# Kernel tuning notes

Hardware: AMD Instinct MI355X
Metric: run time of the kernel (lower is better)

## Reference

```python
import jax, jax.numpy as jnp
import numpy as np

E, EDGE, MEM = 32768, 128, 128
IN = EDGE + 2 * MEM              # 384
HID = 512
NK = 64                          # num_kernels
KNOTS = 16                       # grid_size
ORDER = 3                        # spline order (cubic)
COEF = KNOTS + ORDER             # 19 basis functions per input dim

# Uniform knot grid on [-1, 1], extended by ORDER knots on each side
_H = 2.0 / KNOTS
GRID = (jnp.arange(-ORDER, KNOTS + ORDER + 1, dtype=jnp.float32) * _H - 1.0)


def _b_splines(x, grid):
    """Cox-de Boor B-spline bases. x: [B, IN] -> [B, IN, COEF]."""
    xe = x[..., None]                                   # [B, IN, 1]
    bases = ((xe >= grid[:-1]) & (xe < grid[1:])).astype(x.dtype)
    for p in range(1, ORDER + 1):
        left = (xe - grid[:-(p + 1)]) / (grid[p:-1] - grid[:-(p + 1)])
        right = (grid[p + 1:] - xe) / (grid[p + 1:] - grid[1:-p])
        bases = left * bases[..., :-1] + right * bases[..., 1:]
    return bases                                        # [B, IN, COEF]


def setup_inputs() -> dict:
    key = jax.random.key(0)
    ks = jax.random.split(key, 7)
    z = jax.random.normal(ks[0], (E, EDGE), jnp.float32)
    mem_src = jax.random.normal(ks[1], (E, MEM), jnp.float32)
    mem_dst = jax.random.normal(ks[2], (E, MEM), jnp.float32)
    base_weight = jax.random.normal(ks[3], (HID, IN), jnp.float32) / np.sqrt(IN)
    spline_weight = jax.random.normal(ks[4], (HID, IN, COEF), jnp.float32) * 0.1
    lin_w = jax.random.normal(ks[5], (NK, HID), jnp.float32) / np.sqrt(HID)
    lin_b = jax.random.normal(ks[6], (NK,), jnp.float32) * 0.01
    return {"z": z, "mem_src": mem_src, "mem_dst": mem_dst,
            "base_weight": base_weight, "spline_weight": spline_weight,
            "lin_w": lin_w, "lin_b": lin_b}


def reference(z, mem_src, mem_dst, base_weight, spline_weight, lin_w, lin_b):
    # concat + tanh squashing (inputs into the [-1,1] knot grid), fp32 math
    x = jnp.tanh(jnp.concatenate([z, mem_src, mem_dst], axis=-1)).astype(jnp.float32)
    # KANLinear: base path (silu residual) + spline path
    bases = _b_splines(x, GRID)                          # [E, IN, COEF]
    h = (jnp.dot(jax.nn.silu(x), base_weight.T)
         + jnp.einsum('bik,oik->bo', bases, spline_weight))  # [E, HID]
    h = jnp.tanh(h)                                      # act='tanh'; dropout=0 -> identity
    return jnp.dot(h, lin_w.T) + lin_b                   # [E, NK]
```

## Files before the change

kernel.cpp:

```cpp
#include <hip/hip_runtime.h>
#include <hip/hip_bf16.h>
#include <cstdint>

#define DI __device__ __forceinline__

using bf16x8 = __attribute__((ext_vector_type(8))) short;
using f32x4  = __attribute__((ext_vector_type(4))) float;

constexpr int IN_DIM = 384;
constexpr int HID    = 512;
constexpr int KTOT   = IN_DIM * 20;
constexpr int BM = 64, BN = 256, BK = 160;
constexpr int NSTEP = KTOT / BK;
constexpr int A_STRIDE_B = 320;
constexpr int A_BYTES    = BM * A_STRIDE_B;
constexpr int LDS_BYTES  = 2 * A_BYTES;

DI unsigned short f2bf(float f) {
  union { float f; uint32_t u; } v; v.f = f;
  uint32_t r = (v.u + 0x7FFFu + ((v.u >> 16) & 1u)) >> 16;
  return (unsigned short)r;
}
DI float fast_tanh(float x) {
  float e = __expf(2.0f * x);
  return 1.0f - 2.0f / (e + 1.0f);
}
DI uint32_t swzw(uint32_t L) { return L ^ ((L >> 6) & 0x70u); }

__global__ __launch_bounds__(256) void kpack(const float* __restrict__ bw,
                                             const float* __restrict__ sw,
                                             unsigned short* __restrict__ Wf) {
  int idx = blockIdx.x * 256 + threadIdx.x;
  int o = idx / IN_DIM;
  int i = idx - o * IN_DIM;
  const float* sp = sw + (size_t)idx * 19;
  const uint32_t gq  = (uint32_t)(o >> 4);
  const uint32_t l16o = (uint32_t)(o & 15);
#pragma unroll
  for (int c = 0; c < 20; ++c) {
    int k = i * 20 + c;
    uint32_t q  = (uint32_t)k >> 5;
    uint32_t kr = (uint32_t)k & 31u;
    uint32_t lane = l16o + ((kr >> 3) << 4);
    uint32_t off = (q * 32u + gq) * 512u + lane * 8u + (kr & 7u);
    float v = (c == 0) ? bw[idx] : sp[c - 1];
    Wf[off] = f2bf(v);
  }
}

__global__ __launch_bounds__(256, 4) void kgemm1(const float* __restrict__ z,
                                                 const float* __restrict__ ms,
                                                 const float* __restrict__ md,
                                                 const unsigned short* __restrict__ Wf,
                                                 unsigned short* __restrict__ hout) {
  extern __shared__ char ldsbuf[];

  const int tid  = threadIdx.x;
  const int lane = tid & 63;
  const int wv   = tid >> 6;
  const int wc   = wv & 3;
  const int l16  = lane & 15;
  const int lhi  = lane >> 4;

  int wg = blockIdx.x;
  int id = (wg & 7) * 128 + (wg >> 3);
  const int mblk = id & 511;
  const int nblk = id >> 9;
  const int row0 = mblk * BM;
  const int col0 = nblk * BN;

  const unsigned short* bpt = Wf + (size_t)(nblk * 16 + wc * 4) * 512 + (size_t)lane * 8;

  const int isl = tid & 7;
  const int arow0 = tid >> 3;
  const uint32_t fw = ((uint32_t)arow0 & 7u) << 4;

  const uint32_t fA = (uint32_t)(l16 & 7) << 4;
  const uint32_t rA = (uint32_t)l16 * A_STRIDE_B + (uint32_t)lhi * 16u;

  f32x4 acc[4][4] = {};

  float xv0, xv1;
  {
    const float* xcol = z + isl;
    float x0 = xcol[(size_t)(row0 + arow0) * 128];
    float x1 = xcol[(size_t)(row0 + arow0 + 32) * 128];
#pragma unroll
    for (int r = 0; r < 2; ++r) {
      float x = (r == 0) ? x0 : x1;
      int arow = arow0 + r * 32;
      float xt = fast_tanh(x);
      float tt = (xt + 1.0f) * 8.0f;
      int   m  = (int)tt; m = m > 16 ? 16 : m;
      float u  = tt - (float)m;
      float omu = 1.0f - u;
      float u2 = u * u, u3 = u2 * u;
      float w0 = omu * omu * omu * (1.0f / 6.0f);
      float w1 = (3.0f * u3 - 6.0f * u2 + 4.0f) * (1.0f / 6.0f);
      float w2 = (-3.0f * u3 + 3.0f * u2 + 3.0f * u + 1.0f) * (1.0f / 6.0f);
      float w3 = u3 * (1.0f / 6.0f);
      float sil = xt / (1.0f + __expf(-xt));
      uint32_t base = (uint32_t)arow * A_STRIDE_B + (uint32_t)isl * 40u;
#pragma unroll
      for (int zz = 0; zz < 5; ++zz)
        *(uint64_t*)(ldsbuf + ((base + zz * 8) ^ fw)) = 0ull;
      *(short*)(ldsbuf + (base ^ fw)) = (short)f2bf(sil);
      *(short*)(ldsbuf + ((base + 2u * (m + 1)) ^ fw)) = (short)f2bf(w0);
      *(short*)(ldsbuf + ((base + 2u * (m + 2)) ^ fw)) = (short)f2bf(w1);
      *(short*)(ldsbuf + ((base + 2u * (m + 3)) ^ fw)) = (short)f2bf(w2);
      if (m < 16)
        *(short*)(ldsbuf + ((base + 2u * (m + 4)) ^ fw)) = (short)f2bf(w3);
    }
    const float* xc1 = z + (8 + isl);
    xv0 = xc1[(size_t)(row0 + arow0) * 128];
    xv1 = xc1[(size_t)(row0 + arow0 + 32) * 128];
  }
  __syncthreads();

  for (int s = 0; s < NSTEP; ++s) {
    const uint32_t pc = (uint32_t)(s & 1);
    const uint32_t pn = pc ^ 1u;
    char* An = ldsbuf + pn * (uint32_t)A_BYTES;
    const char* Ac = ldsbuf + pc * (uint32_t)A_BYTES;

    float xn0 = 0.f, xn1 = 0.f;
    if (s + 1 < NSTEP) {
#pragma unroll
      for (int r = 0; r < 2; ++r) {
        float x = (r == 0) ? xv0 : xv1;
        int arow = arow0 + r * 32;
        float xt = fast_tanh(x);
        float tt = (xt + 1.0f) * 8.0f;
        int   m  = (int)tt; m = m > 16 ? 16 : m;
        float u  = tt - (float)m;
        float omu = 1.0f - u;
        float u2 = u * u, u3 = u2 * u;
        float w0 = omu * omu * omu * (1.0f / 6.0f);
        float w1 = (3.0f * u3 - 6.0f * u2 + 4.0f) * (1.0f / 6.0f);
        float w2 = (-3.0f * u3 + 3.0f * u2 + 3.0f * u + 1.0f) * (1.0f / 6.0f);
        float w3 = u3 * (1.0f / 6.0f);
        float sil = xt / (1.0f + __expf(-xt));
        uint32_t base = (uint32_t)arow * A_STRIDE_B + (uint32_t)isl * 40u;
#pragma unroll
        for (int zz = 0; zz < 5; ++zz)
          *(uint64_t*)(An + ((base + zz * 8) ^ fw)) = 0ull;
        *(short*)(An + (base ^ fw)) = (short)f2bf(sil);
        *(short*)(An + ((base + 2u * (m + 1)) ^ fw)) = (short)f2bf(w0);
        *(short*)(An + ((base + 2u * (m + 2)) ^ fw)) = (short)f2bf(w1);
        *(short*)(An + ((base + 2u * (m + 3)) ^ fw)) = (short)f2bf(w2);
        if (m < 16)
          *(short*)(An + ((base + 2u * (m + 4)) ^ fw)) = (short)f2bf(w3);
      }
      if (s + 2 < NSTEP) {
        int i = (s + 2) * 8 + isl;
        const float* src = (i < 128) ? z : (i < 256 ? ms : md);
        const float* xcol = src + (i & 127);
        xn0 = xcol[(size_t)(row0 + arow0) * 128];
        xn1 = xcol[(size_t)(row0 + arow0 + 32) * 128];
      }
    }

    const size_t qoff = (size_t)s * 5u * 16384u;
#pragma unroll
    for (int ks = 0; ks < 5; ++ks) {
      bf16x8 af[4], bfr[4];
#pragma unroll
      for (int ni = 0; ni < 4; ++ni)
        bfr[ni] = *(const bf16x8*)(bpt + qoff + (size_t)ks * 16384u + (size_t)ni * 512u);
#pragma unroll
      for (int mi = 0; mi < 4; ++mi)
        af[mi] = *(const bf16x8*)(Ac + ((rA + (uint32_t)(mi * 16) * A_STRIDE_B + ks * 64u) ^ fA));
#pragma unroll
      for (int mi = 0; mi < 4; ++mi)
#pragma unroll
        for (int ni = 0; ni < 4; ++ni)
          acc[mi][ni] = __builtin_amdgcn_mfma_f32_16x16x32_bf16(af[mi], bfr[ni], acc[mi][ni], 0, 0, 0);
    }

    __syncthreads();
    xv0 = xn0; xv1 = xn1;
  }

#pragma unroll
  for (int mi = 0; mi < 4; ++mi)
#pragma unroll
    for (int ni = 0; ni < 4; ++ni)
#pragma unroll
      for (int rg = 0; rg < 4; ++rg) {
        int grow = row0 + mi * 16 + lhi * 4 + rg;
        int gcol = col0 + wc * 64 + ni * 16 + l16;
        hout[(size_t)grow * HID + gcol] = f2bf(fast_tanh(acc[mi][ni][rg]));
      }
}

__global__ __launch_bounds__(256) void kfinal(const unsigned short* __restrict__ h,
                                              const float* __restrict__ lw,
                                              const float* __restrict__ lb,
                                              float* __restrict__ out) {
  __shared__ unsigned short Ws[64 * 512];
  char* WsB = (char*)Ws;
  const int tid  = threadIdx.x;
  const int lane = tid & 63;
  const int wv   = tid >> 6;
  const int l16  = lane & 15;
  const int lhi  = lane >> 4;
  const int row0 = blockIdx.x * 64;

#pragma unroll
  for (int it = 0; it < 16; ++it) {
    int c = it * 256 + tid;
    int r = c >> 6;
    int k8 = (c & 63) * 8;
    const float* g = lw + r * 512 + k8;
    float4 f0 = *(const float4*)g;
    float4 f1 = *(const float4*)(g + 4);
    union { unsigned short s[8]; bf16x8 v; } u;
    u.s[0] = f2bf(f0.x); u.s[1] = f2bf(f0.y); u.s[2] = f2bf(f0.z); u.s[3] = f2bf(f0.w);
    u.s[4] = f2bf(f1.x); u.s[5] = f2bf(f1.y); u.s[6] = f2bf(f1.z); u.s[7] = f2bf(f1.w);
    *(bf16x8*)(WsB + swzw((uint32_t)r * 1024u + (uint32_t)k8 * 2u)) = u.v;
  }
  __syncthreads();

  const int arow = row0 + wv * 16 + l16;
  const unsigned short* ag = h + (size_t)arow * HID + lhi * 8;
  f32x4 acc[4] = {};
#pragma unroll
  for (int ks = 0; ks < 16; ++ks) {
    bf16x8 af = *(const bf16x8*)(ag + ks * 32);
#pragma unroll
    for (int ni = 0; ni < 4; ++ni) {
      uint32_t L = (uint32_t)(ni * 16 + l16) * 1024u + (uint32_t)(ks * 64 + lhi * 16);
      bf16x8 bfr = *(const bf16x8*)(WsB + swzw(L));
      acc[ni] = __builtin_amdgcn_mfma_f32_16x16x32_bf16(af, bfr, acc[ni], 0, 0, 0);
    }
  }
#pragma unroll
  for (int ni = 0; ni < 4; ++ni) {
    int col = ni * 16 + l16;
    float bias = lb[col];
#pragma unroll
    for (int rg = 0; rg < 4; ++rg) {
      int grow = row0 + wv * 16 + lhi * 4 + rg;
      out[(size_t)grow * 64 + col] = acc[ni][rg] + bias;
    }
  }
}

extern "C" void kernel_launch(void* const* d_in, const int* in_sizes, int n_in,
                              void* d_out, int out_size, void* d_ws, size_t ws_size,
                              hipStream_t stream) {
  const float* z  = (const float*)d_in[0];
  const float* ms = (const float*)d_in[1];
  const float* md = (const float*)d_in[2];
  const float* bw = (const float*)d_in[3];
  const float* sw = (const float*)d_in[4];
  const float* lw = (const float*)d_in[5];
  const float* lb = (const float*)d_in[6];
  float* out = (float*)d_out;

  unsigned short* Wf = (unsigned short*)d_ws;
  unsigned short* hb = (unsigned short*)((char*)d_ws + (8u << 20));

  (void)hipFuncSetAttribute((const void*)kgemm1,
                            hipFuncAttributeMaxDynamicSharedMemorySize, LDS_BYTES);

  kpack<<<(HID * IN_DIM) / 256, 256, 0, stream>>>(bw, sw, Wf);
  kgemm1<<<1024, 256, LDS_BYTES, stream>>>(z, ms, md, Wf, hb);
  kfinal<<<32768 / 64, 256, 0, stream>>>(hb, lw, lb, out);
}
```

Before: 279.3 us.

## Widen GEMM block to full hidden width so spline bases are built once per row

```diff
diff --git a/kernel.cpp b/kernel.cpp
--- a/kernel.cpp
+++ b/kernel.cpp
@@ -10,7 +10,7 @@
 constexpr int IN_DIM = 384;
 constexpr int HID    = 512;
 constexpr int KTOT   = IN_DIM * 20;
-constexpr int BM = 64, BN = 256, BK = 160;
+constexpr int BM = 64, BN = 512, BK = 160;
 constexpr int NSTEP = KTOT / BK;
 constexpr int A_STRIDE_B = 320;
 constexpr int A_BYTES    = BM * A_STRIDE_B;
@@ -48,7 +48,7 @@
   }
 }
 
-__global__ __launch_bounds__(256, 4) void kgemm1(const float* __restrict__ z,
+__global__ __launch_bounds__(512, 4) void kgemm1(const float* __restrict__ z,
                                                  const float* __restrict__ ms,
                                                  const float* __restrict__ md,
                                                  const unsigned short* __restrict__ Wf,
@@ -57,39 +57,62 @@
 
   const int tid  = threadIdx.x;
   const int lane = tid & 63;
-  const int wv   = tid >> 6;
-  const int wc   = wv & 3;
+  const int wc   = tid >> 6;
   const int l16  = lane & 15;
   const int lhi  = lane >> 4;
 
   int wg = blockIdx.x;
-  int id = (wg & 7) * 128 + (wg >> 3);
-  const int mblk = id & 511;
-  const int nblk = id >> 9;
-  const int row0 = mblk * BM;
-  const int col0 = nblk * BN;
-
-  const unsigned short* bpt = Wf + (size_t)(nblk * 16 + wc * 4) * 512 + (size_t)lane * 8;
+  int id = (wg & 7) * 64 + (wg >> 3);
+  const int row0 = id * BM;
+
+  const unsigned short* bpt = Wf + (size_t)(wc * 4) * 512 + (size_t)lane * 8;
 
   const int isl = tid & 7;
-  const int arow0 = tid >> 3;
-  const uint32_t fw = ((uint32_t)arow0 & 7u) << 4;
+  const int arow = tid >> 3;
+  const uint32_t fw = ((uint32_t)arow & 7u) << 4;
+  const uint32_t abase = (uint32_t)arow * A_STRIDE_B + (uint32_t)isl * 40u;
 
   const uint32_t fA = (uint32_t)(l16 & 7) << 4;
   const uint32_t rA = (uint32_t)l16 * A_STRIDE_B + (uint32_t)lhi * 16u;
 
   f32x4 acc[4][4] = {};
 
-  float xv0, xv1;
+  float xv0;
   {
-    const float* xcol = z + isl;
-    float x0 = xcol[(size_t)(row0 + arow0) * 128];
-    float x1 = xcol[(size_t)(row0 + arow0 + 32) * 128];
-#pragma unroll
-    for (int r = 0; r < 2; ++r) {
-      float x = (r == 0) ? x0 : x1;
-      int arow = arow0 + r * 32;
-      float xt = fast_tanh(x);
+    float x = z[(size_t)(row0 + arow) * 128 + isl];
+    float xt = fast_tanh(x);
+    float tt = (xt + 1.0f) * 8.0f;
+    int   m  = (int)tt; m = m > 16 ? 16 : m;
+    float u  = tt - (float)m;
+    float omu = 1.0f - u;
+    float u2 = u * u, u3 = u2 * u;
+    float w0 = omu * omu * omu * (1.0f / 6.0f);
+    float w1 = (3.0f * u3 - 6.0f * u2 + 4.0f) * (1.0f / 6.0f);
+    float w2 = (-3.0f * u3 + 3.0f * u2 + 3.0f * u + 1.0f) * (1.0f / 6.0f);
+    float w3 = u3 * (1.0f / 6.0f);
+    float sil = xt / (1.0f + __expf(-xt));
+#pragma unroll
+    for (int zz = 0; zz < 5; ++zz)
+      *(uint64_t*)(ldsbuf + ((abase + zz * 8) ^ fw)) = 0ull;
+    *(short*)(ldsbuf + (abase ^ fw)) = (short)f2bf(sil);
+    *(short*)(ldsbuf + ((abase + 2u * (m + 1)) ^ fw)) = (short)f2bf(w0);
+    *(short*)(ldsbuf + ((abase + 2u * (m + 2)) ^ fw)) = (short)f2bf(w1);
+    *(short*)(ldsbuf + ((abase + 2u * (m + 3)) ^ fw)) = (short)f2bf(w2);
+    if (m < 16)
+      *(short*)(ldsbuf + ((abase + 2u * (m + 4)) ^ fw)) = (short)f2bf(w3);
+    xv0 = z[(size_t)(row0 + arow) * 128 + 8 + isl];
+  }
+  __syncthreads();
+
+  for (int s = 0; s < NSTEP; ++s) {
+    const uint32_t pc = (uint32_t)(s & 1);
+    const uint32_t pn = pc ^ 1u;
+    char* An = ldsbuf + pn * (uint32_t)A_BYTES;
+    const char* Ac = ldsbuf + pc * (uint32_t)A_BYTES;
+
+    float xn0 = 0.f;
+    if (s + 1 < NSTEP) {
+      float xt = fast_tanh(xv0);
       float tt = (xt + 1.0f) * 8.0f;
       int   m  = (int)tt; m = m > 16 ? 16 : m;
       float u  = tt - (float)m;
@@ -100,63 +123,19 @@
       float w2 = (-3.0f * u3 + 3.0f * u2 + 3.0f * u + 1.0f) * (1.0f / 6.0f);
       float w3 = u3 * (1.0f / 6.0f);
       float sil = xt / (1.0f + __expf(-xt));
-      uint32_t base = (uint32_t)arow * A_STRIDE_B + (uint32_t)isl * 40u;
 #pragma unroll
       for (int zz = 0; zz < 5; ++zz)
-        *(uint64_t*)(ldsbuf + ((base + zz * 8) ^ fw)) = 0ull;
-      *(short*)(ldsbuf + (base ^ fw)) = (short)f2bf(sil);
-      *(short*)(ldsbuf + ((base + 2u * (m + 1)) ^ fw)) = (short)f2bf(w0);
-      *(short*)(ldsbuf + ((base + 2u * (m + 2)) ^ fw)) = (short)f2bf(w1);
-      *(short*)(ldsbuf + ((base + 2u * (m + 3)) ^ fw)) = (short)f2bf(w2);
+        *(uint64_t*)(An + ((abase + zz * 8) ^ fw)) = 0ull;
+      *(short*)(An + (abase ^ fw)) = (short)f2bf(sil);
+      *(short*)(An + ((abase + 2u * (m + 1)) ^ fw)) = (short)f2bf(w0);
+      *(short*)(An + ((abase + 2u * (m + 2)) ^ fw)) = (short)f2bf(w1);
+      *(short*)(An + ((abase + 2u * (m + 3)) ^ fw)) = (short)f2bf(w2);
       if (m < 16)
-        *(short*)(ldsbuf + ((base + 2u * (m + 4)) ^ fw)) = (short)f2bf(w3);
-    }
-    const float* xc1 = z + (8 + isl);
-    xv0 = xc1[(size_t)(row0 + arow0) * 128];
-    xv1 = xc1[(size_t)(row0 + arow0 + 32) * 128];
-  }
-  __syncthreads();
-
-  for (int s = 0; s < NSTEP; ++s) {
-    const uint32_t pc = (uint32_t)(s & 1);
-    const uint32_t pn = pc ^ 1u;
-    char* An = ldsbuf + pn * (uint32_t)A_BYTES;
-    const char* Ac = ldsbuf + pc * (uint32_t)A_BYTES;
-
-    float xn0 = 0.f, xn1 = 0.f;
-    if (s + 1 < NSTEP) {
-#pragma unroll
-      for (int r = 0; r < 2; ++r) {
-        float x = (r == 0) ? xv0 : xv1;
-        int arow = arow0 + r * 32;
-        float xt = fast_tanh(x);
-        float tt = (xt + 1.0f) * 8.0f;
-        int   m  = (int)tt; m = m > 16 ? 16 : m;
-        float u  = tt - (float)m;
-        float omu = 1.0f - u;
-        float u2 = u * u, u3 = u2 * u;
-        float w0 = omu * omu * omu * (1.0f / 6.0f);
-        float w1 = (3.0f * u3 - 6.0f * u2 + 4.0f) * (1.0f / 6.0f);
-        float w2 = (-3.0f * u3 + 3.0f * u2 + 3.0f * u + 1.0f) * (1.0f / 6.0f);
-        float w3 = u3 * (1.0f / 6.0f);
-        float sil = xt / (1.0f + __expf(-xt));
-        uint32_t base = (uint32_t)arow * A_STRIDE_B + (uint32_t)isl * 40u;
-#pragma unroll
-        for (int zz = 0; zz < 5; ++zz)
-          *(uint64_t*)(An + ((base + zz * 8) ^ fw)) = 0ull;
-        *(short*)(An + (base ^ fw)) = (short)f2bf(sil);
-        *(short*)(An + ((base + 2u * (m + 1)) ^ fw)) = (short)f2bf(w0);
-        *(short*)(An + ((base + 2u * (m + 2)) ^ fw)) = (short)f2bf(w1);
-        *(short*)(An + ((base + 2u * (m + 3)) ^ fw)) = (short)f2bf(w2);
-        if (m < 16)
-          *(short*)(An + ((base + 2u * (m + 4)) ^ fw)) = (short)f2bf(w3);
-      }
+        *(short*)(An + ((abase + 2u * (m + 4)) ^ fw)) = (short)f2bf(w3);
       if (s + 2 < NSTEP) {
         int i = (s + 2) * 8 + isl;
         const float* src = (i < 128) ? z : (i < 256 ? ms : md);
-        const float* xcol = src + (i & 127);
-        xn0 = xcol[(size_t)(row0 + arow0) * 128];
-        xn1 = xcol[(size_t)(row0 + arow0 + 32) * 128];
+        xn0 = src[(size_t)(row0 + arow) * 128 + (i & 127)];
       }
     }
 
@@ -178,7 +157,7 @@
     }
 
     __syncthreads();
-    xv0 = xn0; xv1 = xn1;
+    xv0 = xn0;
   }
 
 #pragma unroll
@@ -188,7 +167,7 @@
 #pragma unroll
       for (int rg = 0; rg < 4; ++rg) {
         int grow = row0 + mi * 16 + lhi * 4 + rg;
-        int gcol = col0 + wc * 64 + ni * 16 + l16;
+        int gcol = wc * 64 + ni * 16 + l16;
         hout[(size_t)grow * HID + gcol] = f2bf(fast_tanh(acc[mi][ni][rg]));
       }
 }
@@ -265,6 +244,6 @@
                             hipFuncAttributeMaxDynamicSharedMemorySize, LDS_BYTES);
 
   kpack<<<(HID * IN_DIM) / 256, 256, 0, stream>>>(bw, sw, Wf);
-  kgemm1<<<1024, 256, LDS_BYTES, stream>>>(z, ms, md, Wf, hb);
+  kgemm1<<<512, 512, LDS_BYTES, stream>>>(z, ms, md, Wf, hb);
   kfinal<<<32768 / 64, 256, 0, stream>>>(hb, lw, lb, out);
 }
```

After: 257.0 us. -8.0%, faster.
